# Kernel tuning notes

Hardware: AMD Instinct MI355X
Metric: run time of the kernel (lower is better)

The kernel has to match this reference:

```python
import jax, jax.numpy as jnp
import numpy as np
import math

B, N, C, EV, H = 16, 4096, 256, 64, 8
A_, B_, C_ = 10, 10, 10  # query group sizes a, b, c
TEMP = 0.1


def setup_inputs() -> dict:
    key = jax.random.key(0)
    ks = jax.random.split(key, 24)
    x = jax.random.normal(ks[0], (B, N, C), jnp.float32)
    origin_x = jax.random.normal(ks[1], (B, N, C), jnp.float32)
    evectors = jax.random.normal(ks[2], (B, A_ + B_ + C_, EV), jnp.float32)
    # numv: cumulative node counts; per-graph diff with 3*diff <= N
    diffs = jax.random.randint(ks[3], (B,), 64, N // 3 + 1)
    numv = jnp.concatenate([jnp.zeros((1,), jnp.int32), jnp.cumsum(diffs).astype(jnp.int32)])
    # additive cross mask: valid where position < 3*diff
    pos = jnp.arange(N)
    valid = pos[None, :] < (3 * diffs)[:, None]  # [B, N]
    mask_cross = jnp.where(valid, 0.0, -1e9).astype(jnp.float32)[:, None, :] * jnp.ones((1, A_ + B_ + C_, 1), jnp.float32)
    s = 0.02
    p = lambda k, shp: jax.random.normal(k, shp, jnp.float32) * s
    inp = {
        'x': x, 'origin_x': origin_x, 'evectors': evectors,
        'mask_cross': mask_cross, 'numv': numv,
        'Wq_G': p(ks[4], (C, EV)), 'Wq_D': p(ks[5], (C, EV)), 'Wq_L': p(ks[6], (C, EV)),
        'Wk_G': p(ks[7], (C, C)), 'Wk_D': p(ks[8], (C, C)), 'Wk_L': p(ks[9], (C, C)),
        'Wv_G': p(ks[10], (C, C)), 'bv_G': jnp.zeros((C,), jnp.float32),
        'Wv_D': p(ks[11], (C, C)), 'bv_D': jnp.zeros((C,), jnp.float32),
        'Wv_L': p(ks[12], (C, C)), 'bv_L': jnp.zeros((C,), jnp.float32),
        'Wo': p(ks[13], (C, C)), 'bo': jnp.zeros((C,), jnp.float32),
    }
    return inp


def _forward(x, origin_x, evectors, mask_cross, numv,
             Wq_G, Wq_D, Wq_L, Wk_G, Wk_D, Wk_L,
             Wv_G, bv_G, Wv_D, bv_D, Wv_L, bv_L, Wo, bo):
    dv = C
    dh = dv // H
    nq = A_ + B_ + C_
    # --- query: per-group linear projections on evectors ---
    Q = jnp.concatenate([
        evectors[:, :A_] @ Wq_G.T,
        evectors[:, A_:A_ + B_] @ Wq_D.T,
        evectors[:, A_ + B_:nq] @ Wq_L.T,
    ], axis=1)  # [B, nq, dv]
    # --- ragged K/V construction: group by position vs per-graph diff ---
    diffs = (numv[1:] - numv[:-1]).astype(jnp.int32)  # [B]
    pos = jnp.arange(N)[None, :]  # [1, N]
    d = diffs[:, None]
    g0 = (pos < d).astype(x.dtype)[..., None]
    g1 = ((pos >= d) & (pos < 2 * d)).astype(x.dtype)[..., None]
    g2 = ((pos >= 2 * d) & (pos < 3 * d)).astype(x.dtype)[..., None]
    Kd = g0 * (x @ Wk_G.T) + g1 * (x @ Wk_D.T) + g2 * (x @ Wk_L.T)  # [B, N, dv]
    Vd = (g0 * (origin_x @ Wv_G.T + bv_G)
          + g1 * (origin_x @ Wv_D.T + bv_D)
          + g2 * (origin_x @ Wv_L.T + bv_L))  # [B, N, dv]
    # --- per-head weight decorrelation loss on Q ---
    Qh = Q.reshape(B, nq, H, dh).transpose(2, 0, 1, 3)  # [H, B, nq, dh]
    wd = jnp.asarray(0.0, Q.dtype)
    for lo, sz in ((0, A_), (A_, B_), (A_ + B_, C_)):
        if sz > 1:
            G = Qh[:, :, lo:lo + sz]  # [H, B, sz, dh]
            corr = jnp.einsum('hbik,hbjk->hbij', G, G)
            diff_m = corr - jnp.eye(sz, dtype=Q.dtype)
            fro = jnp.sqrt(jnp.sum(diff_m * diff_m, axis=(-2, -1)))  # [H, B]
            wd = wd + fro.mean(axis=1).sum()
    # --- masked, temperature-scaled multi-head attention ---
    Kh = Kd.reshape(B, N, H, dh)
    Vh = Vd.reshape(B, N, H, dh)
    Qh2 = Q.reshape(B, nq, H, dh)
    scores = jnp.einsum('bqhd,bkhd->bhqk', Qh2, Kh) / (math.sqrt(dv) * TEMP)
    scores = scores + mask_cross[:, None, :, :]
    Aw = jax.nn.softmax(scores, axis=-1)
    out = jnp.einsum('bhqk,bkhd->bqhd', Aw, Vh).reshape(B, nq, dv)
    out = out + jax.nn.relu(out @ Wo.T + bo)
    nrm = jnp.linalg.norm(out, axis=2, keepdims=True)
    out = out / jnp.maximum(nrm, 1e-12)
    return out, wd


def reference(x, origin_x, evectors, mask_cross, numv,
              Wq_G, Wq_D, Wq_L, Wk_G, Wk_D, Wk_L,
              Wv_G, bv_G, Wv_D, bv_D, Wv_L, bv_L, Wo, bo):
    return _forward(x, origin_x, evectors, mask_cross, numv,
                    Wq_G, Wq_D, Wq_L, Wk_G, Wk_D, Wk_L,
                    Wv_G, bv_G, Wv_D, bv_D, Wv_L, bv_L, Wo, bo)
```

## Files before the change

kernel.cpp:

```cpp
#include <hip/hip_runtime.h>
#include <math.h>


typedef __bf16 bf16x8 __attribute__((ext_vector_type(8)));
typedef float  f32x4  __attribute__((ext_vector_type(4)));

namespace {
constexpr int kB   = 16;
constexpr int kN   = 4096;
constexpr int kC   = 256;
constexpr int kEV  = 64;
constexpr int kH   = 8;
constexpr int kDH  = 32;
constexpr int kNQ  = 30;
constexpr int kCHUNK = 64;
constexpr int kNCH = kN / kCHUNK;
constexpr float kScale = 0.625f;
}

__device__ __forceinline__ unsigned short f32_to_bf16(float f) {
  unsigned int u = __float_as_uint(f);
  unsigned int r = (u + 0x7FFFu + ((u >> 16) & 1u)) >> 16;
  return (unsigned short)r;
}
__device__ __forceinline__ f32x4 splat4(float v) {
  f32x4 r; r[0] = v; r[1] = v; r[2] = v; r[3] = v; return r;
}

__global__ __launch_bounds__(256) void prep_kernel(
    const float* __restrict__ ev,
    const float* __restrict__ WqG, const float* __restrict__ WqD,
    const float* __restrict__ WqL,
    const float* __restrict__ WkG, const float* __restrict__ WkD,
    const float* __restrict__ WkL,
    const float* __restrict__ WvG, const float* __restrict__ WvD,
    const float* __restrict__ WvL,
    unsigned short* __restrict__ Wb,
    float* __restrict__ Qw, unsigned short* __restrict__ Qb)
{
  const int bid = blockIdx.x, tid = threadIdx.x;
  __shared__ float e[kEV];
  if (bid < 192) {
    const int mat = bid >> 5;
    const float* src = (mat == 0) ? WkG : (mat == 1) ? WkD : (mat == 2) ? WkL
                     : (mat == 3) ? WvG : (mat == 4) ? WvD : WvL;
    const int i0 = (((bid & 31) << 8) + tid) * 8;
    const float4* s4 = (const float4*)(src + i0);
    float4 a = s4[0], b = s4[1];
    uint4 pack = make_uint4(
        (unsigned int)f32_to_bf16(a.x) | ((unsigned int)f32_to_bf16(a.y) << 16),
        (unsigned int)f32_to_bf16(a.z) | ((unsigned int)f32_to_bf16(a.w) << 16),
        (unsigned int)f32_to_bf16(b.x) | ((unsigned int)f32_to_bf16(b.y) << 16),
        (unsigned int)f32_to_bf16(b.z) | ((unsigned int)f32_to_bf16(b.w) << 16));
    *(uint4*)(Wb + (size_t)mat * 65536 + i0) = pack;
  } else {
    const int idx = bid - 192;
    const int b = idx >> 5, qq = idx & 31;
    if (qq >= kNQ) { Qb[((size_t)(b * 32 + qq)) * kC + tid] = 0; return; }
    if (tid < kEV) e[tid] = ev[((size_t)(b * kNQ + qq)) * kEV + tid];
    __syncthreads();
    const float* W = (qq < 10) ? WqG : (qq < 20) ? WqD : WqL;
    const float4* wr = (const float4*)(W + (size_t)tid * kEV);
    const float4* er = (const float4*)e;
    float s = 0.0f;
#pragma unroll
    for (int j = 0; j < kEV / 4; ++j) {
      float4 w = wr[j], v = er[j];
      s = fmaf(v.x, w.x, s); s = fmaf(v.y, w.y, s);
      s = fmaf(v.z, w.z, s); s = fmaf(v.w, w.w, s);
    }
    Qw[((size_t)(b * kNQ + qq)) * kC + tid] = s;
    Qb[((size_t)(b * 32 + qq)) * kC + tid] = f32_to_bf16(s * kScale);
  }
}

__global__ __launch_bounds__(128) void wd_kernel(
    const float* __restrict__ Qw, float* __restrict__ wdp)
{
  const int g = blockIdx.x >> 3;
  const int h = blockIdx.x & 7;
  const int tid = threadIdx.x;
  const int lo = g * 10;
  __shared__ float sred[128];
  float local = 0.0f;
  for (int b = 0; b < kB; ++b) {
    float v = 0.0f;
    if (tid < 100) {
      int i = tid / 10, j = tid % 10;
      const float* qi = Qw + ((size_t)(b * kNQ + lo + i)) * kC + h * kDH;
      const float* qj = Qw + ((size_t)(b * kNQ + lo + j)) * kC + h * kDH;
      float corr = 0.0f;
#pragma unroll
      for (int k = 0; k < kDH; ++k) corr = fmaf(qi[k], qj[k], corr);
      float diff = corr - (i == j ? 1.0f : 0.0f);
      v = diff * diff;
    }
    sred[tid] = v;
    __syncthreads();
    for (int s2 = 64; s2 > 0; s2 >>= 1) {
      if (tid < s2) sred[tid] += sred[tid + s2];
      __syncthreads();
    }
    if (tid == 0) local += sqrtf(sred[0]);
    __syncthreads();
  }
  if (tid == 0) wdp[blockIdx.x] = local * (1.0f / 16.0f);
}

struct ProjAcc { f32x4 acc[4][2]; f32x4 accX[2]; };

template <bool HASB>
__device__ __forceinline__ void proj_mfma(
    const unsigned short* Xs,
    const unsigned short* W0, const unsigned short* W1,
    const float* __restrict__ bias0, const float* __restrict__ bias1,
    int rsplit, bool two, int wcol0, int lane, ProjAcc& P)
{
  const int lg = lane >> 4, lr = lane & 15;
  const bool strad = two && (rsplit & 15);
  const int ms = rsplit >> 4;

#pragma unroll
  for (int n = 0; n < 2; ++n) {
    float b0v = 0.0f, b1v = 0.0f;
    if constexpr (HASB) {
      b0v = bias0[wcol0 + n * 16 + lr];
      b1v = two ? bias1[wcol0 + n * 16 + lr] : b0v;
    }
#pragma unroll
    for (int m = 0; m < 4; ++m)
      P.acc[m][n] = splat4((m * 16 < rsplit) ? b0v : b1v);
    P.accX[n] = splat4(b1v);
  }

  for (int kt = 0; kt < 8; ++kt) {
    bf16x8 a[4];
#pragma unroll
    for (int m = 0; m < 4; ++m) {
      const int row = m * 16 + lr;
      const int c16 = (kt * 4 + lg) ^ (row & 7);
      a[m] = *reinterpret_cast<const bf16x8*>(Xs + row * kC + c16 * 8);
    }
    bf16x8 ams = a[0];
#pragma unroll
    for (int m = 1; m < 4; ++m) if (m == ms) ams = a[m];

    const int k0 = kt * 32 + lg * 8;
#pragma unroll
    for (int n = 0; n < 2; ++n) {
      const int ct = wcol0 + n * 16 + lr;
      bf16x8 b0 = *reinterpret_cast<const bf16x8*>(W0 + (size_t)ct * kC + k0);
      if (!two) {
#pragma unroll
        for (int m = 0; m < 4; ++m)
          P.acc[m][n] = __builtin_amdgcn_mfma_f32_16x16x32_bf16(a[m], b0, P.acc[m][n], 0, 0, 0);
      } else {
        bf16x8 b1 = *reinterpret_cast<const bf16x8*>(W1 + (size_t)ct * kC + k0);
#pragma unroll
        for (int m = 0; m < 4; ++m) {
          bf16x8 bs = (m * 16 < rsplit) ? b0 : b1;
          P.acc[m][n] = __builtin_amdgcn_mfma_f32_16x16x32_bf16(a[m], bs, P.acc[m][n], 0, 0, 0);
        }
        if (strad)
          P.accX[n] = __builtin_amdgcn_mfma_f32_16x16x32_bf16(ams, b1, P.accX[n], 0, 0, 0);
      }
    }
  }
}

template <bool VT>
__device__ __forceinline__ void proj_store(
    unsigned short* dst, const ProjAcc& P,
    int rsplit, bool two, int wcol0, int lane)
{
  const int lg = lane >> 4, lr = lane & 15;
  const bool strad = two && (rsplit & 15);
  const int ms = rsplit >> 4;
#pragma unroll
  for (int m = 0; m < 4; ++m) {
#pragma unroll
    for (int n = 0; n < 2; ++n) {
      const int col = wcol0 + n * 16 + lr;
      if constexpr (VT) {
        unsigned short us[4];
#pragma unroll
        for (int j = 0; j < 4; ++j) {
          const int row = m * 16 + lg * 4 + j;
          float v = P.acc[m][n][j];
          if (strad && m == ms && row >= rsplit) v = P.accX[n][j];
          us[j] = f32_to_bf16(v);
        }
        const int row0 = m * 16 + lg * 4;
        const int ck = ((row0 >> 3) ^ (col & 7));
        uint2 pk = make_uint2((unsigned int)us[0] | ((unsigned int)us[1] << 16),
                              (unsigned int)us[2] | ((unsigned int)us[3] << 16));
        *(uint2*)(dst + col * kCHUNK + ck * 8 + (row0 & 7)) = pk;
      } else {
#pragma unroll
        for (int j = 0; j < 4; ++j) {
          const int row = m * 16 + lg * 4 + j;
          float v = P.acc[m][n][j];
          if (strad && m == ms && row >= rsplit) v = P.accX[n][j];
          dst[row * kC + (col ^ ((row & 7) << 3))] = f32_to_bf16(v);
        }
      }
    }
  }
}

__global__ __launch_bounds__(512, 4) void chunk_kernel(
    const float* __restrict__ x, const float* __restrict__ ox,
    const int* __restrict__ numv,
    const unsigned short* __restrict__ Wb,
    const float* __restrict__ bvG, const float* __restrict__ bvD,
    const float* __restrict__ bvL,
    const unsigned short* __restrict__ Qb,
    float* __restrict__ Pl, float* __restrict__ Po)
{
  __shared__ unsigned short Xs[kCHUNK * kC];
  __shared__ unsigned short Kl[kCHUNK * kC];

  int nv[17];
#pragma unroll
  for (int i = 0; i < 17; ++i) nv[i] = numv[i];
  int t = blockIdx.x, b = 0, ch = -1;
#pragma unroll
  for (int bb = 0; bb < kB; ++bb) {
    const int lc = (3 * (nv[bb + 1] - nv[bb]) + 63) >> 6;
    if (ch < 0) { if (t < lc) { b = bb; ch = t; } else t -= lc; }
  }
  if (ch < 0) return;

  const int tid = threadIdx.x;
  const int n0 = ch * kCHUNK;
  const int d = nv[b + 1] - nv[b];
  const int limit = 3 * d;
  const int nvalid = min(kCHUNK, limit - n0);

  const int lane = tid & 63, wv = tid >> 6;
  const int lg = lane >> 4, lr = lane & 15;
  const int wcol0 = wv * 32;

  const int g0 = (n0 >= 2 * d) ? 2 : (n0 >= d) ? 1 : 0;
  const int n63 = n0 + 63;
  const int g1 = (n63 >= 2 * d) ? 2 : (n63 >= d) ? 1 : 0;
  const bool two = (g1 != g0);
  const int rsplit = two ? ((g1 == 1 ? d : 2 * d) - n0) : kCHUNK;

  const unsigned short* WkA = Wb + (size_t)g0 * 65536;
  const unsigned short* WkB = Wb + (size_t)g1 * 65536;
  const unsigned short* WvA = Wb + (size_t)(3 + g0) * 65536;
  const unsigned short* WvB = Wb + (size_t)(3 + g1) * 65536;
  const float* bvA = (g0 == 0) ? bvG : (g0 == 1) ? bvD : bvL;
  const float* bvB = (g1 == 0) ? bvG : (g1 == 1) ? bvD : bvL;

  auto stage = [&](const float* __restrict__ src) {
    uint4* dst4 = (uint4*)Xs;
#pragma unroll
    for (int i = 0; i < 4; ++i) {
      const int cid = tid + i * 512;
      const int row = cid >> 5, c5 = cid & 31;
      const float4* g = (const float4*)(src + (size_t)row * kC + c5 * 8);
      float4 w0 = g[0], w1 = g[1];
      unsigned int u0 = ((unsigned int)f32_to_bf16(w0.y) << 16) | f32_to_bf16(w0.x);
      unsigned int u1 = ((unsigned int)f32_to_bf16(w0.w) << 16) | f32_to_bf16(w0.z);
      unsigned int u2 = ((unsigned int)f32_to_bf16(w1.y) << 16) | f32_to_bf16(w1.x);
      unsigned int u3 = ((unsigned int)f32_to_bf16(w1.w) << 16) | f32_to_bf16(w1.z);
      dst4[row * 32 + (c5 ^ (row & 7))] = make_uint4(u0, u1, u2, u3);
    }
  };

  stage(x + ((size_t)b * kN + n0) * kC);
  __syncthreads();
  {
    ProjAcc PK;
    proj_mfma<false>(Xs, WkA, WkB, nullptr, nullptr, rsplit, two, wcol0, lane, PK);
    proj_store<false>(Kl, PK, rsplit, two, wcol0, lane);
  }
  __syncthreads();

  stage(ox + ((size_t)b * kN + n0) * kC);
  __syncthreads();
  ProjAcc PV;
  proj_mfma<true>(Xs, WvA, WvB, bvA, bvB, rsplit, two, wcol0, lane, PV);
  __syncthreads();
  unsigned short* Vt = Xs;
  proj_store<true>(Vt, PV, rsplit, two, wcol0, lane);
  __syncthreads();

  const int h = wv;
  const unsigned short* qrow = Qb + (size_t)b * 32 * kC;
  bf16x8 aq0 = *reinterpret_cast<const bf16x8*>(qrow + lr * kC + h * kDH + lg * 8);
  bf16x8 aq1 = *reinterpret_cast<const bf16x8*>(qrow + (16 + lr) * kC + h * kDH + lg * 8);

  f32x4 s[2][4];
#pragma unroll
  for (int m = 0; m < 2; ++m)
#pragma unroll
    for (int n = 0; n < 4; ++n) s[m][n] = splat4(0.0f);

#pragma unroll
  for (int n = 0; n < 4; ++n) {
    const int row = n * 16 + lr;
    const int c16 = (h * 4 + lg) ^ (row & 7);
    bf16x8 bk = *reinterpret_cast<const bf16x8*>(Kl + row * kC + c16 * 8);
    s[0][n] = __builtin_amdgcn_mfma_f32_16x16x32_bf16(aq0, bk, s[0][n], 0, 0, 0);
    s[1][n] = __builtin_amdgcn_mfma_f32_16x16x32_bf16(aq1, bk, s[1][n], 0, 0, 0);
  }
  __syncthreads();

  unsigned short* Pw = Kl + wv * 2048;
  f32x4 lsum[2];
  lsum[0] = splat4(0.0f); lsum[1] = splat4(0.0f);

#pragma unroll
  for (int m = 0; m < 2; ++m) {
#pragma unroll
    for (int n = 0; n < 4; ++n) {
      const int key = n * 16 + lr;
      const bool kok = key < nvalid;
      f32x4 p;
#pragma unroll
      for (int j = 0; j < 4; ++j) p[j] = kok ? __expf(s[m][n][j]) : 0.0f;
      lsum[m] += p;
#pragma unroll
      for (int j = 0; j < 4; ++j) {
        const int q = m * 16 + lg * 4 + j;
        const int ck = (key >> 3) ^ (q & 7);
        Pw[q * kCHUNK + ck * 8 + (key & 7)] = f32_to_bf16(p[j]);
      }
    }
  }

#pragma unroll
  for (int msk = 1; msk < 16; msk <<= 1) {
#pragma unroll
    for (int m = 0; m < 2; ++m)
#pragma unroll
      for (int j = 0; j < 4; ++j)
        lsum[m][j] += __shfl_xor(lsum[m][j], msk, 16);
  }
  const int plbase = (b * kNCH + ch) * kNQ * kH;
  if (lr == 0) {
#pragma unroll
    for (int m = 0; m < 2; ++m)
#pragma unroll
      for (int j = 0; j < 4; ++j) {
        const int q = m * 16 + lg * 4 + j;
        if (q < kNQ) Pl[plbase + q * kH + h] = lsum[m][j];
      }
  }

  f32x4 o[2][2];
#pragma unroll
  for (int m = 0; m < 2; ++m)
#pragma unroll
    for (int n = 0; n < 2; ++n) o[m][n] = splat4(0.0f);

#pragma unroll
  for (int ks = 0; ks < 2; ++ks) {
    const int ckp = (ks * 4 + lg) ^ (lr & 7);
    bf16x8 ap0 = *reinterpret_cast<const bf16x8*>(Pw + lr * kCHUNK + ckp * 8);
    bf16x8 ap1 = *reinterpret_cast<const bf16x8*>(Pw + (16 + lr) * kCHUNK + ckp * 8);
#pragma unroll
    for (int n = 0; n < 2; ++n) {
      const int c = h * kDH + n * 16 + lr;
      const int ckv = (ks * 4 + lg) ^ (c & 7);
      bf16x8 bv = *reinterpret_cast<const bf16x8*>(Vt + c * kCHUNK + ckv * 8);
      o[0][n] = __builtin_amdgcn_mfma_f32_16x16x32_bf16(ap0, bv, o[0][n], 0, 0, 0);
      o[1][n] = __builtin_amdgcn_mfma_f32_16x16x32_bf16(ap1, bv, o[1][n], 0, 0, 0);
    }
  }

#pragma unroll
  for (int m = 0; m < 2; ++m)
#pragma unroll
    for (int n = 0; n < 2; ++n)
#pragma unroll
      for (int j = 0; j < 4; ++j) {
        const int q = m * 16 + lg * 4 + j;
        if (q < kNQ)
          Po[((size_t)(plbase + q * kH + h)) * kDH + n * 16 + lr] = o[m][n][j];
      }
}

__global__ __launch_bounds__(256) void combine_kernel(
    const float* __restrict__ Pl, const float* __restrict__ Po,
    const int* __restrict__ numv,
    const float* __restrict__ Wo, const float* __restrict__ bo,
    const float* __restrict__ wdp,
    float* __restrict__ out)
{
  const int bq = blockIdx.x;
  const int tid = threadIdx.x;

  if (bq == kB * kNQ) {
    float v = (tid < 24) ? wdp[tid] : 0.0f;
#pragma unroll
    for (int off = 32; off > 0; off >>= 1) v += __shfl_down(v, off);
    if (tid == 0) out[(size_t)kB * kNQ * kC] = v;
    return;
  }

  const int b = bq / kNQ, q = bq % kNQ;
  const int h = tid >> 5, kk = tid & 31;

  const int d = numv[b + 1] - numv[b];
  const int ncv = min(kNCH, (3 * d + kCHUNK - 1) >> 6);

  float l = 0.0f, oacc = 0.0f;
#pragma unroll 4
  for (int ch = 0; ch < ncv; ++ch) {
    const int idx = (b * kNCH + ch) * kNQ * kH + q * kH + h;
    l += Pl[idx];
    oacc += Po[(size_t)idx * kDH + kk];
  }
  const float attn = oacc / l;

  __shared__ float row[kC];
  row[tid] = attn;
  __syncthreads();

  const float4* wr = (const float4*)(Wo + (size_t)tid * kC);
  const float4* rr = (const float4*)row;
  float s = 0.0f;
#pragma unroll
  for (int j = 0; j < kC / 4; ++j) {
    float4 w = wr[j], v = rr[j];
    s = fmaf(v.x, w.x, s); s = fmaf(v.y, w.y, s);
    s = fmaf(v.z, w.z, s); s = fmaf(v.w, w.w, s);
  }
  s += bo[tid];
  const float y = attn + fmaxf(s, 0.0f);

  float v = y * y;
#pragma unroll
  for (int off = 32; off > 0; off >>= 1) v += __shfl_down(v, off);
  __shared__ float red[4];
  if ((tid & 63) == 0) red[tid >> 6] = v;
  __syncthreads();
  const float tot = red[0] + red[1] + red[2] + red[3];
  const float nrm = fmaxf(sqrtf(tot), 1e-12f);
  out[(size_t)bq * kC + tid] = y / nrm;
}

extern "C" void kernel_launch(void* const* d_in, const int* in_sizes, int n_in,
                              void* d_out, int out_size, void* d_ws, size_t ws_size,
                              hipStream_t stream) {
  const float* x    = (const float*)d_in[0];
  const float* ox   = (const float*)d_in[1];
  const float* ev   = (const float*)d_in[2];
  const int*   numv = (const int*)d_in[4];
  const float* WqG  = (const float*)d_in[5];
  const float* WqD  = (const float*)d_in[6];
  const float* WqL  = (const float*)d_in[7];
  const float* WkG  = (const float*)d_in[8];
  const float* WkD  = (const float*)d_in[9];
  const float* WkL  = (const float*)d_in[10];
  const float* WvG  = (const float*)d_in[11];
  const float* bvG  = (const float*)d_in[12];
  const float* WvD  = (const float*)d_in[13];
  const float* bvD  = (const float*)d_in[14];
  const float* WvL  = (const float*)d_in[15];
  const float* bvL  = (const float*)d_in[16];
  const float* Wo   = (const float*)d_in[17];
  const float* bo   = (const float*)d_in[18];

  float* out = (float*)d_out;
  char*  ws  = (char*)d_ws;

  float* Qw = (float*)ws;
  unsigned short* Qb = (unsigned short*)(ws + 491520);
  unsigned short* Wb = (unsigned short*)(ws + 491520 + 262144);
  float* Pl  = (float*)(ws + 1540096);
  float* Po  = (float*)(ws + 1540096 + 983040);
  float* wdp = (float*)(ws + 1540096 + 983040 + 31457280);

  prep_kernel<<<704, 256, 0, stream>>>(ev, WqG, WqD, WqL,
                                       WkG, WkD, WkL, WvG, WvD, WvL,
                                       Wb, Qw, Qb);
  wd_kernel<<<24, 128, 0, stream>>>(Qw, wdp);
  chunk_kernel<<<kB * kNCH, 512, 0, stream>>>(
      x, ox, numv, Wb, bvG, bvD, bvL, Qb, Pl, Po);
  combine_kernel<<<kB * kNQ + 1, 256, 0, stream>>>(Pl, Po, numv, Wo, bo, wdp, out);
}
```

Measured before the change: 110.0 us.

## Load activations directly from global into MFMA operands and fold wd into chunk kernel

The K and V projections now read fp32 activations straight from global memory, converting them to bf16 in registers, instead of first staging each chunk into swizzled LDS. This drops the staging pass and several barriers. The cost is that each wave re-reads the same rows from global or cache with less coalesced access. The separate wd kernel also becomes the first 24 blocks of the chunk kernel, removing one launch, and the split K/V LDS buffers keep total LDS the same.

Result: slower. 162.4 us (+47.6%).

```diff
diff --git a/kernel.cpp b/kernel.cpp
--- a/kernel.cpp
+++ b/kernel.cpp
@@ -74,45 +74,12 @@
   }
 }
 
-__global__ __launch_bounds__(128) void wd_kernel(
-    const float* __restrict__ Qw, float* __restrict__ wdp)
-{
-  const int g = blockIdx.x >> 3;
-  const int h = blockIdx.x & 7;
-  const int tid = threadIdx.x;
-  const int lo = g * 10;
-  __shared__ float sred[128];
-  float local = 0.0f;
-  for (int b = 0; b < kB; ++b) {
-    float v = 0.0f;
-    if (tid < 100) {
-      int i = tid / 10, j = tid % 10;
-      const float* qi = Qw + ((size_t)(b * kNQ + lo + i)) * kC + h * kDH;
-      const float* qj = Qw + ((size_t)(b * kNQ + lo + j)) * kC + h * kDH;
-      float corr = 0.0f;
-#pragma unroll
-      for (int k = 0; k < kDH; ++k) corr = fmaf(qi[k], qj[k], corr);
-      float diff = corr - (i == j ? 1.0f : 0.0f);
-      v = diff * diff;
-    }
-    sred[tid] = v;
-    __syncthreads();
-    for (int s2 = 64; s2 > 0; s2 >>= 1) {
-      if (tid < s2) sred[tid] += sred[tid + s2];
-      __syncthreads();
-    }
-    if (tid == 0) local += sqrtf(sred[0]);
-    __syncthreads();
-  }
-  if (tid == 0) wdp[blockIdx.x] = local * (1.0f / 16.0f);
-}
-
 struct ProjAcc { f32x4 acc[4][2]; f32x4 accX[2]; };
 
 template <bool HASB>
-__device__ __forceinline__ void proj_mfma(
-    const unsigned short* Xs,
-    const unsigned short* W0, const unsigned short* W1,
+__device__ __forceinline__ void proj_mfma_g(
+    const float* __restrict__ X,
+    const unsigned short* __restrict__ W0, const unsigned short* __restrict__ W1,
     const float* __restrict__ bias0, const float* __restrict__ bias1,
     int rsplit, bool two, int wcol0, int lane, ProjAcc& P)
 {
@@ -133,13 +100,17 @@
     P.accX[n] = splat4(b1v);
   }
 
+#pragma unroll
   for (int kt = 0; kt < 8; ++kt) {
     bf16x8 a[4];
 #pragma unroll
     for (int m = 0; m < 4; ++m) {
-      const int row = m * 16 + lr;
-      const int c16 = (kt * 4 + lg) ^ (row & 7);
-      a[m] = *reinterpret_cast<const bf16x8*>(Xs + row * kC + c16 * 8);
+      const float4* p = (const float4*)(X + (size_t)(m * 16 + lr) * kC + kt * 32 + lg * 8);
+      float4 v0 = p[0], v1 = p[1];
+      bf16x8 t;
+      t[0] = (__bf16)v0.x; t[1] = (__bf16)v0.y; t[2] = (__bf16)v0.z; t[3] = (__bf16)v0.w;
+      t[4] = (__bf16)v1.x; t[5] = (__bf16)v1.y; t[6] = (__bf16)v1.z; t[7] = (__bf16)v1.w;
+      a[m] = t;
     }
     bf16x8 ams = a[0];
 #pragma unroll
@@ -215,15 +186,49 @@
     const float* __restrict__ bvG, const float* __restrict__ bvD,
     const float* __restrict__ bvL,
     const unsigned short* __restrict__ Qb,
-    float* __restrict__ Pl, float* __restrict__ Po)
+    const float* __restrict__ Qw,
+    float* __restrict__ Pl, float* __restrict__ Po, float* __restrict__ wdp)
 {
-  __shared__ unsigned short Xs[kCHUNK * kC];
   __shared__ unsigned short Kl[kCHUNK * kC];
+  __shared__ unsigned short Vt[kC * kCHUNK];
+
+  const int tid = threadIdx.x;
+
+  if (blockIdx.x < 24) {
+    const int g = blockIdx.x >> 3;
+    const int h = blockIdx.x & 7;
+    const int lo = g * 10;
+    float* sred = (float*)Kl;
+    float local = 0.0f;
+    for (int b = 0; b < kB; ++b) {
+      float v = 0.0f;
+      if (tid < 100) {
+        int i = tid / 10, j = tid % 10;
+        const float* qi = Qw + ((size_t)(b * kNQ + lo + i)) * kC + h * kDH;
+        const float* qj = Qw + ((size_t)(b * kNQ + lo + j)) * kC + h * kDH;
+        float corr = 0.0f;
+#pragma unroll
+        for (int k = 0; k < kDH; ++k) corr = fmaf(qi[k], qj[k], corr);
+        float diff = corr - (i == j ? 1.0f : 0.0f);
+        v = diff * diff;
+      }
+      sred[tid] = v;
+      __syncthreads();
+      for (int s2 = 256; s2 > 0; s2 >>= 1) {
+        if (tid < s2) sred[tid] += sred[tid + s2];
+        __syncthreads();
+      }
+      if (tid == 0) local += sqrtf(sred[0]);
+      __syncthreads();
+    }
+    if (tid == 0) wdp[blockIdx.x] = local * (1.0f / 16.0f);
+    return;
+  }
 
   int nv[17];
 #pragma unroll
   for (int i = 0; i < 17; ++i) nv[i] = numv[i];
-  int t = blockIdx.x, b = 0, ch = -1;
+  int t = blockIdx.x - 24, b = 0, ch = -1;
 #pragma unroll
   for (int bb = 0; bb < kB; ++bb) {
     const int lc = (3 * (nv[bb + 1] - nv[bb]) + 63) >> 6;
@@ -231,7 +236,6 @@
   }
   if (ch < 0) return;
 
-  const int tid = threadIdx.x;
   const int n0 = ch * kCHUNK;
   const int d = nv[b + 1] - nv[b];
   const int limit = 3 * d;
@@ -254,38 +258,19 @@
   const float* bvA = (g0 == 0) ? bvG : (g0 == 1) ? bvD : bvL;
   const float* bvB = (g1 == 0) ? bvG : (g1 == 1) ? bvD : bvL;
 
-  auto stage = [&](const float* __restrict__ src) {
-    uint4* dst4 = (uint4*)Xs;
-#pragma unroll
-    for (int i = 0; i < 4; ++i) {
-      const int cid = tid + i * 512;
-      const int row = cid >> 5, c5 = cid & 31;
-      const float4* g = (const float4*)(src + (size_t)row * kC + c5 * 8);
-      float4 w0 = g[0], w1 = g[1];
-      unsigned int u0 = ((unsigned int)f32_to_bf16(w0.y) << 16) | f32_to_bf16(w0.x);
-      unsigned int u1 = ((unsigned int)f32_to_bf16(w0.w) << 16) | f32_to_bf16(w0.z);
-      unsigned int u2 = ((unsigned int)f32_to_bf16(w1.y) << 16) | f32_to_bf16(w1.x);
-      unsigned int u3 = ((unsigned int)f32_to_bf16(w1.w) << 16) | f32_to_bf16(w1.z);
-      dst4[row * 32 + (c5 ^ (row & 7))] = make_uint4(u0, u1, u2, u3);
-    }
-  };
-
-  stage(x + ((size_t)b * kN + n0) * kC);
-  __syncthreads();
   {
     ProjAcc PK;
-    proj_mfma<false>(Xs, WkA, WkB, nullptr, nullptr, rsplit, two, wcol0, lane, PK);
+    proj_mfma_g<false>(x + ((size_t)b * kN + n0) * kC, WkA, WkB,
+                       nullptr, nullptr, rsplit, two, wcol0, lane, PK);
     proj_store<false>(Kl, PK, rsplit, two, wcol0, lane);
   }
-  __syncthreads();
-
-  stage(ox + ((size_t)b * kN + n0) * kC);
-  __syncthreads();
-  ProjAcc PV;
-  proj_mfma<true>(Xs, WvA, WvB, bvA, bvB, rsplit, two, wcol0, lane, PV);
-  __syncthreads();
-  unsigned short* Vt = Xs;
-  proj_store<true>(Vt, PV, rsplit, two, wcol0, lane);
+
+  {
+    ProjAcc PV;
+    proj_mfma_g<true>(ox + ((size_t)b * kN + n0) * kC, WvA, WvB,
+                      bvA, bvB, rsplit, two, wcol0, lane, PV);
+    proj_store<true>(Vt, PV, rsplit, two, wcol0, lane);
+  }
   __syncthreads();
 
   const int h = wv;
@@ -479,8 +464,7 @@
   prep_kernel<<<704, 256, 0, stream>>>(ev, WqG, WqD, WqL,
                                        WkG, WkD, WkL, WvG, WvD, WvL,
                                        Wb, Qw, Qb);
-  wd_kernel<<<24, 128, 0, stream>>>(Qw, wdp);
-  chunk_kernel<<<kB * kNCH, 512, 0, stream>>>(
-      x, ox, numv, Wb, bvG, bvD, bvL, Qb, Pl, Po);
+  chunk_kernel<<<24 + kB * kNCH, 512, 0, stream>>>(
+      x, ox, numv, Wb, bvG, bvD, bvL, Qb, Qw, Pl, Po, wdp);
   combine_kernel<<<kB * kNQ + 1, 256, 0, stream>>>(Pl, Po, numv, Wo, bo, wdp, out);
 }
```
